# Kernel tuning notes

Hardware: AMD Instinct MI355X
Metric: run time of the kernel (lower is better)

## Reference

```python
import jax, jax.numpy as jnp
import numpy as np

# Fixed-shape Conformer chunked attention (Gemma3n audio style)
S = 8192          # seq_len
H = 16            # num_heads
D = 128           # head_dim
HD = H * D        # hidden size = 2048
C = 12            # chunk_size
MP = 12           # max_past_horizon
MF = 0            # max_future_horizon
CTX = C + MP + MF # context_size = 24
POS = MP + MF + 1 # pos_length = 13
N = (S + C - 1) // C            # num_blocks
PAD = N * C - S                 # pad_amount
Q_SCALE = D ** -0.5 * 1.4426950408889634  # head_dim**-0.5 / softplus(0)
SOFTCAP = 50.0


def setup_inputs() -> dict:
    key = jax.random.key(0)
    ks = jax.random.split(key, 8)
    w = lambda k, shape: jax.random.normal(k, shape, jnp.float32) * 0.02
    return {
        "hidden_states": jax.random.normal(ks[0], (1, S, HD), jnp.float32),
        "position_embeddings": jax.random.normal(ks[1], (POS, HD), jnp.float32),
        "Wq": w(ks[2], (HD, HD)),
        "Wk": w(ks[3], (HD, HD)),
        "Wv": w(ks[4], (HD, HD)),
        "W_rel": w(ks[5], (HD, HD)),
        "W_post": w(ks[6], (HD, HD)),
        "per_dim_scale": jax.random.normal(ks[7], (D,), jnp.float32) * 0.1,
    }


def reference(hidden_states, position_embeddings, Wq, Wk, Wv, W_rel, W_post, per_dim_scale):
    x = hidden_states[0]  # [S, HD]
    q = (x @ Wq).reshape(S, H, D) * (Q_SCALE * jax.nn.softplus(per_dim_scale))
    k = (x @ Wk).reshape(S, H, D)  # k_scale = 1.0
    v = (x @ Wv).reshape(S, H, D)

    # query blocks [N, C, H, D]
    qb = jnp.pad(q, ((0, PAD), (0, 0), (0, 0))).reshape(N, C, H, D)
    # key/value padded then gathered into sliding context blocks [N, CTX, H, D]
    kp = jnp.pad(k, ((MP, MF + C - 1), (0, 0), (0, 0)))
    vp = jnp.pad(v, ((MP, MF + C - 1), (0, 0), (0, 0)))
    idx = jnp.arange(N)[:, None] * C + jnp.arange(CTX)[None, :]  # [N, CTX]
    kb = kp[idx]
    vb = vp[idx]

    rel_k = (position_embeddings @ W_rel).reshape(POS, H, D)

    # content scores [H, N, C, CTX]
    ac = jnp.einsum('nchd,nkhd->hnck', qb, kb)
    # relative-position scores via shift trick
    bd = jnp.einsum('nchd,phd->hncp', qb, rel_k)          # [H, N, C, POS]
    bd = jnp.pad(bd, ((0, 0), (0, 0), (0, 0), (0, CTX + 1 - POS)))
    bd = bd.reshape(H, N, C * (CTX + 1))[:, :, :C * CTX].reshape(H, N, C, CTX)

    attn = jnp.tanh((ac + bd) / SOFTCAP) * SOFTCAP        # softcap
    attn = jax.nn.softmax(attn, axis=-1)

    out = jnp.einsum('hnck,nkhd->nchd', attn, vb).reshape(N * C, HD)[:S]
    return (out @ W_post)[None]  # [1, S, HD]
```

## Files before the change

kernel.cpp:

```cpp
#include <hip/hip_runtime.h>
#include <hip/hip_bf16.h>

#define S_LEN 8192
#define NH    16
#define HD    128
#define HID   2048
#define NQKV  6144
#define CHUNK 12
#define MP    12
#define CTX   24
#define POS   13
#define NBLK  683

typedef short bf16x8 __attribute__((ext_vector_type(8)));
typedef float f32x4  __attribute__((ext_vector_type(4)));
typedef unsigned short u16;
typedef u16 u16x8 __attribute__((ext_vector_type(8)));
typedef u16 u16x4 __attribute__((ext_vector_type(4)));

#define MFMA16 __builtin_amdgcn_mfma_f32_16x16x32_bf16

__device__ __forceinline__ void glds16(const u16* g, u16* l) {
  __builtin_amdgcn_global_load_lds(
      (__attribute__((address_space(1))) void*)(void*)g,
      (__attribute__((address_space(3))) void*)l, 16, 0, 0);
}

__device__ __forceinline__ u16 f2b(float f) {
  __hip_bfloat16 h = __float2bfloat16(f);
  return *(u16*)&h;
}

__global__ __launch_bounds__(256) void f32_to_bf16(const float* __restrict__ in,
                                                   u16* __restrict__ out, int n) {
  int i = (blockIdx.x * 256 + threadIdx.x) * 4;
  if (i < n) {
    float4 v = *(const float4*)(in + i);
    u16x4 o = {f2b(v.x), f2b(v.y), f2b(v.z), f2b(v.w)};
    *(u16x4*)(out + i) = o;
  }
}

__global__ __launch_bounds__(256) void transpose4(const float* __restrict__ W0,
                                                  const float* __restrict__ W1,
                                                  const float* __restrict__ W2,
                                                  const float* __restrict__ W3,
                                                  u16* __restrict__ out) {
  __shared__ u16 t[64][72];
  const int z = blockIdx.z;
  const float* in = (z == 0) ? W0 : (z == 1) ? W1 : (z == 2) ? W2 : W3;
  u16* dst = out + (size_t)z * HID * HID;
  const int bx = blockIdx.x * 64, by = blockIdx.y * 64;
  const int x = threadIdx.x & 63;
  const int y4 = threadIdx.x >> 6;
  for (int r = y4; r < 64; r += 4)
    t[r][x] = f2b(in[(size_t)(by + r) * HID + bx + x]);
  __syncthreads();
  for (int r = y4; r < 64; r += 4)
    dst[(size_t)(bx + r) * HID + by + x] = t[x][r];
}

__global__ void qscale_kernel(const float* __restrict__ pds, float* __restrict__ qs) {
  int d = threadIdx.x;
  float x = pds[d];
  float sp = log1pf(expf(x));
  qs[d] = 0.08838834764831845f * 1.4426950408889634f * sp;
}

__global__ __launch_bounds__(256) void relk_atomic(const float* __restrict__ pos,
                                                   const float* __restrict__ Wrel,
                                                   float* __restrict__ RELF) {
  const int col = blockIdx.x * 256 + threadIdx.x;
  const int c0 = blockIdx.y * 256;
  float acc[POS] = {};
  for (int c = c0; c < c0 + 256; ++c) {
    float wv = Wrel[(size_t)c * HID + col];
#pragma unroll
    for (int p = 0; p < POS; ++p) acc[p] += pos[p * HID + c] * wv;
  }
#pragma unroll
  for (int p = 0; p < POS; ++p) atomicAdd(&RELF[p * HID + col], acc[p]);
}

__global__ __launch_bounds__(256) void relk_cvt(const float* __restrict__ RELF,
                                                u16* __restrict__ REL) {
  int i = blockIdx.x * 256 + threadIdx.x;
  if (i < POS * HID) REL[i] = f2b(RELF[i]);
}

__global__ __launch_bounds__(256) void gemm_bt(const u16* __restrict__ A,
                                               const u16* __restrict__ Bt,
                                               u16* __restrict__ Co,
                                               float* __restrict__ Cf,
                                               const float* __restrict__ colscale,
                                               int NN, int csLimit) {
  __shared__ u16 lA[2][128 * 32];
  __shared__ u16 lB[2][128 * 32];
  const int tid = threadIdx.x;
  const int lane = tid & 63, w = tid >> 6;
  const int quad = lane >> 4, l = lane & 15;
  const int bm = blockIdx.x * 128, bn = blockIdx.y * 128;
  const int wm = (w >> 1) * 64, wn = (w & 1) * 64;

  f32x4 acc[4][4] = {};

  for (int kt = 0; kt < HID; kt += 64) {
#pragma unroll
    for (int r = 0; r < 2; ++r) {
      int o = w * 1024 + r * 4096 + lane * 16;
      int m = o >> 6;
      int ke = (o & 63) >> 1;
      const u16* ga = A + (size_t)(bm + m) * HID + kt + ke;
      const u16* gb = Bt + (size_t)(bn + m) * HID + kt + ke;
      u16* dA = lA[0] + w * 512 + r * 2048;
      u16* dB = lB[0] + w * 512 + r * 2048;
      glds16(ga, dA);
      glds16(ga + 32, dA + 128 * 32);
      glds16(gb, dB);
      glds16(gb + 32, dB + 128 * 32);
    }
    __syncthreads();

#pragma unroll
    for (int kk = 0; kk < 2; ++kk) {
      bf16x8 af[4], bfr[4];
#pragma unroll
      for (int i = 0; i < 4; ++i)
        af[i] = *(const bf16x8*)(lA[kk] + (wm + i * 16 + l) * 32 + quad * 8);
#pragma unroll
      for (int j = 0; j < 4; ++j)
        bfr[j] = *(const bf16x8*)(lB[kk] + (wn + j * 16 + l) * 32 + quad * 8);
#pragma unroll
      for (int i = 0; i < 4; ++i)
#pragma unroll
        for (int j = 0; j < 4; ++j)
          acc[i][j] = MFMA16(af[i], bfr[j], acc[i][j], 0, 0, 0);
    }
    __syncthreads();
  }

#pragma unroll
  for (int i = 0; i < 4; ++i)
#pragma unroll
    for (int j = 0; j < 4; ++j)
#pragma unroll
      for (int r = 0; r < 4; ++r) {
        int row = bm + wm + i * 16 + quad * 4 + r;
        int col = bn + wn + j * 16 + l;
        float v = acc[i][j][r];
        if (colscale && col < csLimit) v *= colscale[col & (HD - 1)];
        if (Cf) Cf[(size_t)row * NN + col] = v;
        else    Co[(size_t)row * NN + col] = f2b(v);
      }
}

__global__ __launch_bounds__(64) void attn_kernel(const u16* __restrict__ qkv,
                                                  const u16* __restrict__ relg,
                                                  u16* __restrict__ og) {
  __shared__ u16 vt[128 * 40];
  __shared__ u16 ps[16 * 40];
  const int n = blockIdx.x, h = blockIdx.y;
  const int lane = threadIdx.x;
  const int quad = lane >> 4, l = lane & 15;
  const int base = n * CHUNK;
  const u16x8 zero8 = {0, 0, 0, 0, 0, 0, 0, 0};

  const u16* qg = qkv + h * HD;
  const u16* kg = qkv + 2048 + h * HD;
  const u16* vg = qkv + 4096 + h * HD;

  const int vctx = lane & 31, vdc = lane >> 5;
#pragma unroll
  for (int i = 0; i < 8; ++i) {
    int dc = vdc + 2 * i;
    int s = base + vctx - MP;
    u16x8 v = (vctx < CTX && s >= 0 && s < S_LEN)
                  ? *(const u16x8*)(vg + (size_t)s * NQKV + dc * 8)
                  : zero8;
#pragma unroll
    for (int jj = 0; jj < 8; ++jj) vt[(dc * 8 + jj) * 40 + vctx] = v[jj];
  }

  const int sq = min(base + l, S_LEN - 1);
  const int sk0 = base + l - MP;
  const int sk1 = base + 4 + l;
  const bool k0v = (sk0 >= 0) && (sk0 < S_LEN);
  const bool k1v = (l < CTX - 16) && (sk1 < S_LEN);
  const u16* qrow = qg + (size_t)sq * NQKV;
  const u16* k0row = kg + (size_t)(k0v ? sk0 : 0) * NQKV;
  const u16* k1row = kg + (size_t)(k1v ? sk1 : 0) * NQKV;
  const u16* rrow = relg + (size_t)(l < POS ? l : 0) * HID + h * HD;

  f32x4 ac0 = {0, 0, 0, 0}, ac1 = {0, 0, 0, 0}, bd = {0, 0, 0, 0};
#pragma unroll
  for (int t = 0; t < 4; ++t) {
    int d0 = t * 32 + quad * 8;
    bf16x8 aQ = *(const bf16x8*)(qrow + d0);
    bf16x8 bK0 = k0v ? *(const bf16x8*)(k0row + d0) : (bf16x8)zero8;
    bf16x8 bK1 = k1v ? *(const bf16x8*)(k1row + d0) : (bf16x8)zero8;
    bf16x8 bR = (l < POS) ? *(const bf16x8*)(rrow + d0) : (bf16x8)zero8;
    ac0 = MFMA16(aQ, bK0, ac0, 0, 0, 0);
    ac1 = MFMA16(aQ, bK1, ac1, 0, 0, 0);
    bd = MFMA16(aQ, bR, bd, 0, 0, 0);
  }

  float p0[4], p1[4];
#pragma unroll
  for (int r = 0; r < 4; ++r) {
    int c = quad * 4 + r;
    int pi0 = l - c;
    int pi1 = 16 + l - c;
    int sp0 = pi0 < 0 ? 0 : (pi0 > 15 ? 15 : pi0);
    int sp1 = pi1 < 0 ? 0 : (pi1 > 15 ? 15 : pi1);
    float b0 = __shfl(bd[r], quad * 16 + sp0, 64);
    float b1 = __shfl(bd[r], quad * 16 + sp1, 64);
    b0 = (pi0 >= 0 && pi0 < POS) ? b0 : 0.0f;
    b1 = (pi1 >= 0 && pi1 < POS) ? b1 : 0.0f;
    float s0 = tanhf((ac0[r] + b0) * (1.0f / 50.0f)) * 50.0f;
    float s1 = tanhf((ac1[r] + b1) * (1.0f / 50.0f)) * 50.0f;
    bool v1 = (l < (CTX - 16));
    if (!v1) s1 = -1e30f;
    float mx = fmaxf(s0, s1);
#pragma unroll
    for (int d = 1; d < 16; d <<= 1) mx = fmaxf(mx, __shfl_xor(mx, d, 64));
    float e0 = __expf(s0 - mx);
    float e1 = v1 ? __expf(s1 - mx) : 0.0f;
    float sm = e0 + e1;
#pragma unroll
    for (int d = 1; d < 16; d <<= 1) sm += __shfl_xor(sm, d, 64);
    float inv = 1.0f / sm;
    p0[r] = e0 * inv;
    p1[r] = e1 * inv;
  }
#pragma unroll
  for (int r = 0; r < 4; ++r) {
    int c = quad * 4 + r;
    ps[c * 40 + l] = f2b(p0[r]);
    ps[c * 40 + 16 + l] = f2b(p1[r]);
  }
  __syncthreads();

  bf16x8 aP = *(const bf16x8*)(ps + l * 40 + quad * 8);
#pragma unroll
  for (int nt = 0; nt < 8; ++nt) {
    bf16x8 bV = *(const bf16x8*)(vt + (nt * 16 + l) * 40 + quad * 8);
    f32x4 o = {0, 0, 0, 0};
    o = MFMA16(aP, bV, o, 0, 0, 0);
#pragma unroll
    for (int r = 0; r < 4; ++r) {
      int c = quad * 4 + r;
      int s = base + c;
      if (c < CHUNK && s < S_LEN)
        og[(size_t)s * HID + h * HD + nt * 16 + l] = f2b(o[r]);
    }
  }
}

extern "C" void kernel_launch(void* const* d_in, const int* in_sizes, int n_in,
                              void* d_out, int out_size, void* d_ws, size_t ws_size,
                              hipStream_t stream) {
  const float* x = (const float*)d_in[0];
  const float* pos = (const float*)d_in[1];
  const float* Wq = (const float*)d_in[2];
  const float* Wk = (const float*)d_in[3];
  const float* Wv = (const float*)d_in[4];
  const float* Wrel = (const float*)d_in[5];
  const float* Wpost = (const float*)d_in[6];
  const float* pds = (const float*)d_in[7];

  char* ws = (char*)d_ws;
  u16* WT  = (u16*)(ws);
  u16* xb  = (u16*)(ws + 33554432);
  u16* AO  = xb;
  u16* QKV = (u16*)(ws + 67108864);
  float* RELF = (float*)(ws + 167772160);
  u16* REL = (u16*)(ws + 167878656);
  float* QS = (float*)(ws + 167931904);

  const int NX = S_LEN * HID;
  f32_to_bf16<<<NX / 4 / 256, 256, 0, stream>>>(x, xb, NX);

  transpose4<<<dim3(32, 32, 4), 256, 0, stream>>>(Wq, Wk, Wv, Wpost, WT);
  qscale_kernel<<<1, 128, 0, stream>>>(pds, QS);

  hipMemsetAsync(RELF, 0, POS * HID * sizeof(float), stream);
  relk_atomic<<<dim3(8, 8), 256, 0, stream>>>(pos, Wrel, RELF);
  relk_cvt<<<(POS * HID + 255) / 256, 256, 0, stream>>>(RELF, REL);

  gemm_bt<<<dim3(64, 48), 256, 0, stream>>>(xb, WT, QKV, nullptr, QS, NQKV, 2048);

  attn_kernel<<<dim3(NBLK, NH), 64, 0, stream>>>(QKV, REL, AO);

  gemm_bt<<<dim3(64, 16), 256, 0, stream>>>(AO, WT + (size_t)3 * HID * HID,
                                            nullptr, (float*)d_out, nullptr, HID, 0);
}
```

Measured before the change: 638.9 us.

## Fuse prep kernels, drop atomics for rel-k, and share V tile across 4 chunks

Merges the x conversion and the weight transposes into one prep launch. It replaces the memset plus atomic rel-k reduction with partial sums followed by a reduce kernel, and folds the q-scale computation into that reduce kernel. The attention kernel now runs 4 waves per block, covering 4 adjacent chunks of one head, and loads a shared 60-row V window once into LDS instead of reloading overlapping context per chunk. This cuts launch count and redundant V traffic, at the cost of larger LDS use and a block-wide sync.

```diff
diff --git a/kernel.cpp b/kernel.cpp
--- a/kernel.cpp
+++ b/kernel.cpp
@@ -13,6 +13,7 @@
 #define NBLK  683
 
 typedef short bf16x8 __attribute__((ext_vector_type(8)));
+typedef short bf16x4 __attribute__((ext_vector_type(4)));
 typedef float f32x4  __attribute__((ext_vector_type(4)));
 typedef unsigned short u16;
 typedef u16 u16x8 __attribute__((ext_vector_type(8)));
@@ -31,61 +32,71 @@
   return *(u16*)&h;
 }
 
-__global__ __launch_bounds__(256) void f32_to_bf16(const float* __restrict__ in,
-                                                   u16* __restrict__ out, int n) {
-  int i = (blockIdx.x * 256 + threadIdx.x) * 4;
-  if (i < n) {
-    float4 v = *(const float4*)(in + i);
-    u16x4 o = {f2b(v.x), f2b(v.y), f2b(v.z), f2b(v.w)};
-    *(u16x4*)(out + i) = o;
-  }
-}
-
-__global__ __launch_bounds__(256) void transpose4(const float* __restrict__ W0,
-                                                  const float* __restrict__ W1,
-                                                  const float* __restrict__ W2,
-                                                  const float* __restrict__ W3,
-                                                  u16* __restrict__ out) {
+__global__ __launch_bounds__(256) void prep(const float* __restrict__ x,
+                                            const float* __restrict__ W0,
+                                            const float* __restrict__ W1,
+                                            const float* __restrict__ W2,
+                                            const float* __restrict__ W3,
+                                            u16* __restrict__ WT,
+                                            u16* __restrict__ xb) {
   __shared__ u16 t[64][72];
-  const int z = blockIdx.z;
-  const float* in = (z == 0) ? W0 : (z == 1) ? W1 : (z == 2) ? W2 : W3;
-  u16* dst = out + (size_t)z * HID * HID;
-  const int bx = blockIdx.x * 64, by = blockIdx.y * 64;
-  const int x = threadIdx.x & 63;
-  const int y4 = threadIdx.x >> 6;
-  for (int r = y4; r < 64; r += 4)
-    t[r][x] = f2b(in[(size_t)(by + r) * HID + bx + x]);
-  __syncthreads();
-  for (int r = y4; r < 64; r += 4)
-    dst[(size_t)(bx + r) * HID + by + x] = t[x][r];
-}
-
-__global__ void qscale_kernel(const float* __restrict__ pds, float* __restrict__ qs) {
-  int d = threadIdx.x;
-  float x = pds[d];
-  float sp = log1pf(expf(x));
-  qs[d] = 0.08838834764831845f * 1.4426950408889634f * sp;
-}
-
-__global__ __launch_bounds__(256) void relk_atomic(const float* __restrict__ pos,
-                                                   const float* __restrict__ Wrel,
-                                                   float* __restrict__ RELF) {
+  const int bid = blockIdx.x;
+  if (bid < 4096) {
+    const int z = bid >> 10, rem = bid & 1023;
+    const float* in = (z == 0) ? W0 : (z == 1) ? W1 : (z == 2) ? W2 : W3;
+    u16* dst = WT + (size_t)z * HID * HID;
+    const int bx = (rem & 31) * 64, by = (rem >> 5) * 64;
+    const int xx = threadIdx.x & 63;
+    const int y4 = threadIdx.x >> 6;
+    for (int r = y4; r < 64; r += 4)
+      t[r][xx] = f2b(in[(size_t)(by + r) * HID + bx + xx]);
+    __syncthreads();
+    for (int r = y4; r < 64; r += 4)
+      dst[(size_t)(bx + r) * HID + by + xx] = t[xx][r];
+  } else {
+    const int cb = bid - 4096;
+#pragma unroll
+    for (int k = 0; k < 4; ++k) {
+      size_t i = ((size_t)cb * 1024 + k * 256 + threadIdx.x) * 4;
+      float4 v = *(const float4*)(x + i);
+      u16x4 o = {f2b(v.x), f2b(v.y), f2b(v.z), f2b(v.w)};
+      *(u16x4*)(xb + i) = o;
+    }
+  }
+}
+
+__global__ __launch_bounds__(256) void relk_part(const float* __restrict__ pos,
+                                                 const float* __restrict__ Wrel,
+                                                 float* __restrict__ RELP) {
   const int col = blockIdx.x * 256 + threadIdx.x;
-  const int c0 = blockIdx.y * 256;
+  const int c0 = blockIdx.y * 512;
   float acc[POS] = {};
-  for (int c = c0; c < c0 + 256; ++c) {
+  for (int c = c0; c < c0 + 512; ++c) {
     float wv = Wrel[(size_t)c * HID + col];
 #pragma unroll
     for (int p = 0; p < POS; ++p) acc[p] += pos[p * HID + c] * wv;
   }
 #pragma unroll
-  for (int p = 0; p < POS; ++p) atomicAdd(&RELF[p * HID + col], acc[p]);
-}
-
-__global__ __launch_bounds__(256) void relk_cvt(const float* __restrict__ RELF,
-                                                u16* __restrict__ REL) {
+  for (int p = 0; p < POS; ++p)
+    RELP[((size_t)blockIdx.y * POS + p) * HID + col] = acc[p];
+}
+
+__global__ __launch_bounds__(256) void relk_red(const float* __restrict__ RELP,
+                                                u16* __restrict__ REL,
+                                                const float* __restrict__ pds,
+                                                float* __restrict__ qs) {
+  if (blockIdx.x == 104) {
+    if (threadIdx.x < HD) {
+      float v = pds[threadIdx.x];
+      float sp = log1pf(expf(v));
+      qs[threadIdx.x] = 0.08838834764831845f * 1.4426950408889634f * sp;
+    }
+    return;
+  }
   int i = blockIdx.x * 256 + threadIdx.x;
-  if (i < POS * HID) REL[i] = f2b(RELF[i]);
+  float s = RELP[i] + RELP[POS * HID + i] + RELP[2 * POS * HID + i] +
+            RELP[3 * POS * HID + i];
+  REL[i] = f2b(s);
 }
 
 __global__ __launch_bounds__(256) void gemm_bt(const u16* __restrict__ A,
@@ -154,32 +165,39 @@
       }
 }
 
-__global__ __launch_bounds__(64) void attn_kernel(const u16* __restrict__ qkv,
-                                                  const u16* __restrict__ relg,
-                                                  u16* __restrict__ og) {
-  __shared__ u16 vt[128 * 40];
-  __shared__ u16 ps[16 * 40];
-  const int n = blockIdx.x, h = blockIdx.y;
-  const int lane = threadIdx.x;
+__global__ __launch_bounds__(256) void attn_kernel(const u16* __restrict__ qkv,
+                                                   const u16* __restrict__ relg,
+                                                   u16* __restrict__ og) {
+  __shared__ u16 vt[128 * 72];
+  __shared__ u16 ps[4][16 * 40];
+  const int tid = threadIdx.x;
+  const int wid = tid >> 6, lane = tid & 63;
   const int quad = lane >> 4, l = lane & 15;
-  const int base = n * CHUNK;
+  const int h = blockIdx.y;
+  const int blockbase = blockIdx.x * 4 * CHUNK;
   const u16x8 zero8 = {0, 0, 0, 0, 0, 0, 0, 0};
 
   const u16* qg = qkv + h * HD;
   const u16* kg = qkv + 2048 + h * HD;
   const u16* vg = qkv + 4096 + h * HD;
 
-  const int vctx = lane & 31, vdc = lane >> 5;
-#pragma unroll
-  for (int i = 0; i < 8; ++i) {
-    int dc = vdc + 2 * i;
-    int s = base + vctx - MP;
-    u16x8 v = (vctx < CTX && s >= 0 && s < S_LEN)
-                  ? *(const u16x8*)(vg + (size_t)s * NQKV + dc * 8)
-                  : zero8;
-#pragma unroll
-    for (int jj = 0; jj < 8; ++jj) vt[(dc * 8 + jj) * 40 + vctx] = v[jj];
-  }
+#pragma unroll
+  for (int i = 0; i < 5; ++i) {
+    int id = tid + 256 * i;
+    if (id < 1152) {
+      int dc = id / 72, j = id - dc * 72;
+      int s = blockbase - 12 + j;
+      u16x8 v = (j < 60 && s >= 0 && s < S_LEN)
+                    ? *(const u16x8*)(vg + (size_t)s * NQKV + dc * 8)
+                    : zero8;
+#pragma unroll
+      for (int jj = 0; jj < 8; ++jj) vt[(dc * 8 + jj) * 72 + j] = v[jj];
+    }
+  }
+  __syncthreads();
+
+  const int base = blockbase + wid * CHUNK;
+  u16* psw = &ps[wid][0];
 
   const int sq = min(base + l, S_LEN - 1);
   const int sk0 = base + l - MP;
@@ -235,15 +253,18 @@
 #pragma unroll
   for (int r = 0; r < 4; ++r) {
     int c = quad * 4 + r;
-    ps[c * 40 + l] = f2b(p0[r]);
-    ps[c * 40 + 16 + l] = f2b(p1[r]);
-  }
-  __syncthreads();
-
-  bf16x8 aP = *(const bf16x8*)(ps + l * 40 + quad * 8);
+    psw[c * 40 + l] = f2b(p0[r]);
+    psw[c * 40 + 16 + l] = f2b(p1[r]);
+  }
+
+  bf16x8 aP = *(const bf16x8*)(psw + l * 40 + quad * 8);
+  const int vcol = 12 * wid + quad * 8;
 #pragma unroll
   for (int nt = 0; nt < 8; ++nt) {
-    bf16x8 bV = *(const bf16x8*)(vt + (nt * 16 + l) * 40 + quad * 8);
+    const u16* vb = vt + (nt * 16 + l) * 72 + vcol;
+    bf16x4 b0 = *(const bf16x4*)(vb);
+    bf16x4 b1 = *(const bf16x4*)(vb + 4);
+    bf16x8 bV = {b0[0], b0[1], b0[2], b0[3], b1[0], b1[1], b1[2], b1[3]};
     f32x4 o = {0, 0, 0, 0};
     o = MFMA16(aP, bV, o, 0, 0, 0);
 #pragma unroll
@@ -273,23 +294,17 @@
   u16* xb  = (u16*)(ws + 33554432);
   u16* AO  = xb;
   u16* QKV = (u16*)(ws + 67108864);
-  float* RELF = (float*)(ws + 167772160);
-  u16* REL = (u16*)(ws + 167878656);
-  float* QS = (float*)(ws + 167931904);
-
-  const int NX = S_LEN * HID;
-  f32_to_bf16<<<NX / 4 / 256, 256, 0, stream>>>(x, xb, NX);
-
-  transpose4<<<dim3(32, 32, 4), 256, 0, stream>>>(Wq, Wk, Wv, Wpost, WT);
-  qscale_kernel<<<1, 128, 0, stream>>>(pds, QS);
-
-  hipMemsetAsync(RELF, 0, POS * HID * sizeof(float), stream);
-  relk_atomic<<<dim3(8, 8), 256, 0, stream>>>(pos, Wrel, RELF);
-  relk_cvt<<<(POS * HID + 255) / 256, 256, 0, stream>>>(RELF, REL);
+  float* RELP = (float*)(ws + 167772160);
+  u16* REL = (u16*)(ws + 168198144);
+  float* QS = (float*)(ws + 168251392);
+
+  prep<<<8192, 256, 0, stream>>>(x, Wq, Wk, Wv, Wpost, WT, xb);
+  relk_part<<<dim3(8, 4), 256, 0, stream>>>(pos, Wrel, RELP);
+  relk_red<<<105, 256, 0, stream>>>(RELP, REL, pds, QS);
 
   gemm_bt<<<dim3(64, 48), 256, 0, stream>>>(xb, WT, QKV, nullptr, QS, NQKV, 2048);
 
-  attn_kernel<<<dim3(NBLK, NH), 64, 0, stream>>>(QKV, REL, AO);
+  attn_kernel<<<dim3(171, 16), 256, 0, stream>>>(QKV, REL, AO);
 
   gemm_bt<<<dim3(64, 16), 256, 0, stream>>>(AO, WT + (size_t)3 * HID * HID,
                                             nullptr, (float*)d_out, nullptr, HID, 0);
```

Result: slower. 686.2 us (+7.4%).
